# Kernel optimization log

Measured on AMD Instinct MI355X. Metric: run time of the kernel, lower is better.

The kernel has to match this reference:

```python
import jax, jax.numpy as jnp
import numpy as np

NUM_TOKENS = 2048  # = token_limit(0.5) * seq_len(4096)


def setup_inputs() -> dict:
    key = jax.random.key(0)
    k0, k1, k2, k3 = jax.random.split(key, 4)
    B, S, D, F = 4, 4096, 2048, 8192
    return {
        "x": jax.random.normal(k0, (B, S, D), dtype=jnp.float32),
        "Wp": jax.random.normal(k1, (D, 1), dtype=jnp.float32) * (1.0 / np.sqrt(D)),
        "bp": jnp.zeros((1,), dtype=jnp.float32),
        "W1": jax.random.normal(k2, (D, F), dtype=jnp.float32) * (1.0 / np.sqrt(D)),
        "b1": jnp.zeros((F,), dtype=jnp.float32),
        "W2": jax.random.normal(k3, (F, D), dtype=jnp.float32) * (1.0 / np.sqrt(F)),
        "b2": jnp.zeros((D,), dtype=jnp.float32),
    }


def reference(x, Wp, bp, W1, b1, W2, b2):
    # Router: per-token scalar score via Linear(dim, 1)
    weights = x @ Wp + bp                      # [B, S, 1]
    # Faithful to source: softmax over dim=-1 (size-1 axis -> all ones)
    weights = jax.nn.softmax(weights, axis=-1)  # [B, S, 1]
    scores = weights[..., 0]                   # [B, S]
    # top-k token selection along the sequence axis
    _, idx = jax.lax.top_k(scores, NUM_TOKENS)  # [B, k] int32
    # gather the selected full tokens (intended semantics of the expand+gather)
    topk_tokens = jnp.take_along_axis(x, idx[:, :, None], axis=1)  # [B, k, D]
    # downstream block: transformer FFN
    h = jax.nn.gelu(topk_tokens @ W1 + b1)     # [B, k, 4D]
    out = h @ W2 + b2                          # [B, k, D]
    return out
```

## Files before the change

### kernel.cpp

```cpp
#include <hip/hip_runtime.h>
#include <hip/hip_bf16.h>

typedef unsigned int u32;
typedef unsigned short u16;

using bf16x8 = __attribute__((ext_vector_type(8))) short;
using f32x4  = __attribute__((ext_vector_type(4))) float;

#define DEVI static __device__ __forceinline__

DEVI u16 f2bf(float f) {
  __hip_bfloat16 h = __float2bfloat16(f);
  union { __hip_bfloat16 h; u16 u; } v; v.h = h;
  return v.u;
}

__global__ void k_convert_x(const float* __restrict__ x, u16* __restrict__ xb) {
  int idx = blockIdx.x * blockDim.x + threadIdx.x;
  size_t e = (size_t)idx * 4;
  int row = (int)(e >> 11);
  int d   = (int)(e & 2047);
  int b = row >> 11, t = row & 2047;
  const float4 v = *reinterpret_cast<const float4*>(
      x + ((size_t)(b * 4096 + t) * 2048 + d));
  ushort4 o;
  o.x = f2bf(v.x); o.y = f2bf(v.y); o.z = f2bf(v.z); o.w = f2bf(v.w);
  *reinterpret_cast<ushort4*>(xb + (size_t)row * 2048 + d) = o;
}

__global__ void k_transpose_bf16(const float* __restrict__ in,
                                 u16* __restrict__ out, int R, int C) {
  __shared__ u16 lds[64][66];
  const int t = threadIdx.x;
  const int tile_r = blockIdx.y * 64;
  const int tile_c = blockIdx.x * 64;
  const int cc = (t & 15) * 4;
  const int r0 = t >> 4;
#pragma unroll
  for (int i = 0; i < 4; ++i) {
    int r = r0 + i * 16;
    const float4 v = *reinterpret_cast<const float4*>(
        in + (size_t)(tile_r + r) * C + tile_c + cc);
    lds[r][cc]     = f2bf(v.x);
    lds[r][cc + 1] = f2bf(v.y);
    lds[r][cc + 2] = f2bf(v.z);
    lds[r][cc + 3] = f2bf(v.w);
  }
  __syncthreads();
  const int rr = (t & 15) * 4;
  const int c0 = t >> 4;
#pragma unroll
  for (int i = 0; i < 4; ++i) {
    int c = c0 + i * 16;
    ushort4 o;
    o.x = lds[rr][c]; o.y = lds[rr + 1][c];
    o.z = lds[rr + 2][c]; o.w = lds[rr + 3][c];
    *reinterpret_cast<ushort4*>(out + (size_t)(tile_c + c) * R + tile_r + rr) = o;
  }
}

#define GLDS16(g, l)                                                          \
  __builtin_amdgcn_global_load_lds(                                           \
      (const __attribute__((address_space(1))) u32*)(g),                      \
      (__attribute__((address_space(3))) u32*)(l), 16, 0, 0)

#define MFMA_GATE()                                                           \
  do {                                                                        \
    asm volatile("s_waitcnt lgkmcnt(0)" ::: "memory");                        \
    __builtin_amdgcn_sched_barrier(0);                                        \
  } while (0)

template <int DO_GELU>
__global__ __launch_bounds__(512, 2) void k_gemm8(
    const u16* __restrict__ A, const u16* __restrict__ B,
    const float* __restrict__ bias, void* __restrict__ Cout,
    int M, int N, int K, int nbn) {
  __shared__ __align__(64) u16 lds[65536];

  const int nwg = gridDim.x;
  const int bid = blockIdx.x;
  const int wg  = (bid & 7) * (nwg >> 3) + (bid >> 3);
  const int bm = wg / nbn, bn = wg % nbn;

  const int tid  = threadIdx.x;
  const int w    = tid >> 6, lane = tid & 63;
  const int wr   = w >> 2, wcol = w & 3;
  const int l15  = lane & 15, lhi = lane >> 4;

  const size_t arow0 = (size_t)bm * 256;
  const size_t brow0 = (size_t)bn * 256;

  const int srow  = tid >> 3;
  const int scolb = ((tid & 7) * 16) ^ ((srow & 7) << 4);
  const u16* pA = A + (arow0 + srow) * (size_t)K + (scolb >> 1);
  const u16* pB = B + (brow0 + srow) * (size_t)K + (scolb >> 1);
  const int wA = w * 512;

  const u32 arow_b = (u32)((wr * 128 + l15) * 128);
  const u32 brow_b = (u32)((wcol * 64 + l15) * 128);
  const u32 axor   = (u32)((lhi * 16) ^ ((l15 & 7) << 4));
  const char* ldsb = (const char*)lds;

  f32x4 acc[8][4] = {};
  const int nk = K >> 6;

#define STAGE_PAIR(KT, PB, C)                                                 \
  do {                                                                        \
    GLDS16(pA + (size_t)(KT) * 64 + (size_t)(C) * 64 * (size_t)K,             \
           lds + (PB) * 16384 + (C) * 4096 + wA);                             \
    GLDS16(pB + (size_t)(KT) * 64 + (size_t)(C) * 64 * (size_t)K,             \
           lds + 32768 + (PB) * 16384 + (C) * 4096 + wA);                     \
  } while (0)

#define READ_A(MH, ABASE)                                                     \
  _Pragma("unroll") for (int m2 = 0; m2 < 4; ++m2)                            \
  _Pragma("unroll") for (int kk = 0; kk < 2; ++kk)                            \
    afr[m2][kk] = *(const bf16x8*)(ldsb + (ABASE) + arow_b +                  \
                                   ((MH)*4 + m2) * 2048 + (axor ^ (kk << 6)));

#define READ_B(DST, NH, BBASE)                                                \
  _Pragma("unroll") for (int n2 = 0; n2 < 2; ++n2)                            \
  _Pragma("unroll") for (int kk = 0; kk < 2; ++kk)                            \
    DST[n2][kk] = *(const bf16x8*)(ldsb + (BBASE) + brow_b +                  \
                                   ((NH)*2 + n2) * 2048 + (axor ^ (kk << 6)));

#define MFMA_Q(MH, NH, BREG)                                                  \
  _Pragma("unroll") for (int m2 = 0; m2 < 4; ++m2)                            \
  _Pragma("unroll") for (int n2 = 0; n2 < 2; ++n2)                            \
  _Pragma("unroll") for (int kk = 0; kk < 2; ++kk)                            \
    acc[(MH)*4 + m2][(NH)*2 + n2] = __builtin_amdgcn_mfma_f32_16x16x32_bf16(  \
        afr[m2][kk], BREG[n2][kk], acc[(MH)*4 + m2][(NH)*2 + n2], 0, 0, 0);

  STAGE_PAIR(0, 0, 0); STAGE_PAIR(0, 0, 1);
  STAGE_PAIR(0, 0, 2); STAGE_PAIR(0, 0, 3);
  if (nk > 1) {
    STAGE_PAIR(1, 1, 0); STAGE_PAIR(1, 1, 1);
    asm volatile("s_waitcnt vmcnt(4)" ::: "memory");
  } else {
    asm volatile("s_waitcnt vmcnt(0)" ::: "memory");
  }
  __builtin_amdgcn_s_barrier();

  for (int kt = 0; kt < nk; ++kt) {
    const int p = kt & 1;
    const u32 abase = (u32)p * 32768u;
    const u32 bbase = 65536u + (u32)p * 32768u;
    bf16x8 afr[4][2], b0[2][2], b1[2][2];

    READ_A(0, abase);
    READ_B(b0, 0, bbase);
    if (kt + 1 < nk) STAGE_PAIR(kt + 1, p ^ 1, 2);
    asm volatile("s_waitcnt lgkmcnt(8)" ::: "memory");
    __builtin_amdgcn_s_barrier();
    MFMA_GATE();
    __builtin_amdgcn_s_setprio(1);
    MFMA_Q(0, 0, b0);
    __builtin_amdgcn_s_setprio(0);
    __builtin_amdgcn_s_barrier();

    READ_B(b1, 1, bbase);
    if (kt + 1 < nk) STAGE_PAIR(kt + 1, p ^ 1, 3);
    __builtin_amdgcn_s_barrier();
    MFMA_GATE();
    __builtin_amdgcn_s_setprio(1);
    MFMA_Q(0, 1, b1);
    __builtin_amdgcn_s_setprio(0);
    __builtin_amdgcn_s_barrier();

    READ_A(1, abase);
    __builtin_amdgcn_s_barrier();
    MFMA_GATE();
    __builtin_amdgcn_s_setprio(1);
    MFMA_Q(1, 1, b1);
    __builtin_amdgcn_s_setprio(0);
    __builtin_amdgcn_s_barrier();

    __builtin_amdgcn_s_setprio(1);
    MFMA_Q(1, 0, b0);
    __builtin_amdgcn_s_setprio(0);
    __builtin_amdgcn_s_barrier();

    if (kt + 2 < nk) {
      STAGE_PAIR(kt + 2, p, 0); STAGE_PAIR(kt + 2, p, 1);
      asm volatile("s_waitcnt vmcnt(4)" ::: "memory");
    } else {
      asm volatile("s_waitcnt vmcnt(0)" ::: "memory");
    }
    __builtin_amdgcn_s_barrier();
  }

#pragma unroll
  for (int m = 0; m < 8; ++m) {
    const int row = (int)arow0 + wr * 128 + m * 16 + lhi * 4;
#pragma unroll
    for (int n = 0; n < 4; ++n) {
      const int col = (int)brow0 + wcol * 64 + n * 16 + l15;
      const float bb = bias[col];
#pragma unroll
      for (int r = 0; r < 4; ++r) {
        float v = acc[m][n][r] + bb;
        if (DO_GELU) {
          float u2 = v * (1.5957691216f + 0.0713548162f * v * v);
          float g  = v / (1.f + __expf(-u2));
          ((u16*)Cout)[(size_t)(row + r) * N + col] = f2bf(g);
        } else {
          ((float*)Cout)[(size_t)(row + r) * N + col] = v;
        }
      }
    }
  }
#undef STAGE_PAIR
#undef READ_A
#undef READ_B
#undef MFMA_Q
}

extern "C" void kernel_launch(void* const* d_in, const int* in_sizes, int n_in,
                              void* d_out, int out_size, void* d_ws,
                              size_t ws_size, hipStream_t stream) {
  const float* x  = (const float*)d_in[0];
  const float* W1 = (const float*)d_in[3];
  const float* b1 = (const float*)d_in[4];
  const float* W2 = (const float*)d_in[5];
  const float* b2 = (const float*)d_in[6];
  float* out = (float*)d_out;

  char* ws = (char*)d_ws;
  u16* Xb  = (u16*)(ws);
  u16* W1T = (u16*)(ws + 33554432);
  u16* W2T = (u16*)(ws + 67108864);
  u16* H   = (u16*)(ws + 100663296);

  k_convert_x<<<16384, 256, 0, stream>>>(x, Xb);
  k_transpose_bf16<<<dim3(8192 / 64, 2048 / 64), 256, 0, stream>>>(W1, W1T, 2048, 8192);
  k_transpose_bf16<<<dim3(2048 / 64, 8192 / 64), 256, 0, stream>>>(W2, W2T, 8192, 2048);
  k_gemm8<1><<<1024, 512, 0, stream>>>(Xb, W1T, b1, (void*)H, 8192, 8192, 2048, 32);
  k_gemm8<0><<<256, 512, 0, stream>>>(H, W2T, b2, (void*)out, 8192, 2048, 8192, 8);
}
```

Before: 562.7 us.

## Prefetch next k-tile fragments during last MFMA quadrant of GEMM loop

```diff
diff --git a/kernel.cpp b/kernel.cpp
--- a/kernel.cpp
+++ b/kernel.cpp
@@ -112,10 +112,10 @@
            lds + 32768 + (PB) * 16384 + (C) * 4096 + wA);                     \
   } while (0)
 
-#define READ_A(MH, ABASE)                                                     \
+#define READ_A(DST, MH, ABASE)                                                \
   _Pragma("unroll") for (int m2 = 0; m2 < 4; ++m2)                            \
   _Pragma("unroll") for (int kk = 0; kk < 2; ++kk)                            \
-    afr[m2][kk] = *(const bf16x8*)(ldsb + (ABASE) + arow_b +                  \
+    DST[m2][kk] = *(const bf16x8*)(ldsb + (ABASE) + arow_b +                  \
                                    ((MH)*4 + m2) * 2048 + (axor ^ (kk << 6)));
 
 #define READ_B(DST, NH, BBASE)                                                \
@@ -124,67 +124,64 @@
     DST[n2][kk] = *(const bf16x8*)(ldsb + (BBASE) + brow_b +                  \
                                    ((NH)*2 + n2) * 2048 + (axor ^ (kk << 6)));
 
-#define MFMA_Q(MH, NH, BREG)                                                  \
+#define MFMA_Q(MH, NH, AREG, BREG)                                            \
   _Pragma("unroll") for (int m2 = 0; m2 < 4; ++m2)                            \
   _Pragma("unroll") for (int n2 = 0; n2 < 2; ++n2)                            \
   _Pragma("unroll") for (int kk = 0; kk < 2; ++kk)                            \
     acc[(MH)*4 + m2][(NH)*2 + n2] = __builtin_amdgcn_mfma_f32_16x16x32_bf16(  \
-        afr[m2][kk], BREG[n2][kk], acc[(MH)*4 + m2][(NH)*2 + n2], 0, 0, 0);
+        AREG[m2][kk], BREG[n2][kk], acc[(MH)*4 + m2][(NH)*2 + n2], 0, 0, 0);
+
+  bf16x8 aL[4][2], aH[4][2], b0[2][2], b1[2][2];
 
   STAGE_PAIR(0, 0, 0); STAGE_PAIR(0, 0, 1);
   STAGE_PAIR(0, 0, 2); STAGE_PAIR(0, 0, 3);
-  if (nk > 1) {
-    STAGE_PAIR(1, 1, 0); STAGE_PAIR(1, 1, 1);
-    asm volatile("s_waitcnt vmcnt(4)" ::: "memory");
-  } else {
-    asm volatile("s_waitcnt vmcnt(0)" ::: "memory");
-  }
+  asm volatile("s_waitcnt vmcnt(0)" ::: "memory");
   __builtin_amdgcn_s_barrier();
+  __builtin_amdgcn_sched_barrier(0);
+  READ_A(aL, 0, 0u);
+  READ_B(b0, 0, 65536u);
 
   for (int kt = 0; kt < nk; ++kt) {
     const int p = kt & 1;
-    const u32 abase = (u32)p * 32768u;
-    const u32 bbase = 65536u + (u32)p * 32768u;
-    bf16x8 afr[4][2], b0[2][2], b1[2][2];
-
-    READ_A(0, abase);
-    READ_B(b0, 0, bbase);
-    if (kt + 1 < nk) STAGE_PAIR(kt + 1, p ^ 1, 2);
-    asm volatile("s_waitcnt lgkmcnt(8)" ::: "memory");
+    const u32 abase  = (u32)p * 32768u;
+    const u32 bbase  = 65536u + (u32)p * 32768u;
+    const u32 nabase = (u32)(p ^ 1) * 32768u;
+    const u32 nbbase = 65536u + (u32)(p ^ 1) * 32768u;
+
+    if (kt + 1 < nk) { STAGE_PAIR(kt + 1, p ^ 1, 0); STAGE_PAIR(kt + 1, p ^ 1, 1); }
     __builtin_amdgcn_s_barrier();
     MFMA_GATE();
     __builtin_amdgcn_s_setprio(1);
-    MFMA_Q(0, 0, b0);
+    MFMA_Q(0, 0, aL, b0);
     __builtin_amdgcn_s_setprio(0);
     __builtin_amdgcn_s_barrier();
 
     READ_B(b1, 1, bbase);
-    if (kt + 1 < nk) STAGE_PAIR(kt + 1, p ^ 1, 3);
+    if (kt + 1 < nk) { STAGE_PAIR(kt + 1, p ^ 1, 2); STAGE_PAIR(kt + 1, p ^ 1, 3); }
     __builtin_amdgcn_s_barrier();
     MFMA_GATE();
     __builtin_amdgcn_s_setprio(1);
-    MFMA_Q(0, 1, b1);
-    __builtin_amdgcn_s_setprio(0);
-    __builtin_amdgcn_s_barrier();
-
-    READ_A(1, abase);
+    MFMA_Q(0, 1, aL, b1);
+    __builtin_amdgcn_s_setprio(0);
+    __builtin_amdgcn_s_barrier();
+
+    READ_A(aH, 1, abase);
     __builtin_amdgcn_s_barrier();
     MFMA_GATE();
     __builtin_amdgcn_s_setprio(1);
-    MFMA_Q(1, 1, b1);
-    __builtin_amdgcn_s_setprio(0);
-    __builtin_amdgcn_s_barrier();
-
-    __builtin_amdgcn_s_setprio(1);
-    MFMA_Q(1, 0, b0);
-    __builtin_amdgcn_s_setprio(0);
-    __builtin_amdgcn_s_barrier();
-
-    if (kt + 2 < nk) {
-      STAGE_PAIR(kt + 2, p, 0); STAGE_PAIR(kt + 2, p, 1);
-      asm volatile("s_waitcnt vmcnt(4)" ::: "memory");
-    } else {
-      asm volatile("s_waitcnt vmcnt(0)" ::: "memory");
+    MFMA_Q(1, 1, aH, b1);
+    __builtin_amdgcn_s_setprio(0);
+    __builtin_amdgcn_s_barrier();
+
+    asm volatile("s_waitcnt vmcnt(0)" ::: "memory");
+    __builtin_amdgcn_s_barrier();
+    __builtin_amdgcn_sched_barrier(0);
+    __builtin_amdgcn_s_setprio(1);
+    MFMA_Q(1, 0, aH, b0);
+    __builtin_amdgcn_s_setprio(0);
+    if (kt + 1 < nk) {
+      READ_A(aL, 0, nabase);
+      READ_B(b0, 0, nbbase);
     }
     __builtin_amdgcn_s_barrier();
   }
```

After: 598.1 us. 6.3% more time.
